# Performance work log

Hardware: AMD Instinct MI355X
Metric: run time of the kernel (lower is better)

Reference implementation:

```python
import jax, jax.numpy as jnp
import numpy as np
import math

B, S, D, H = 2, 2048, 1024, 16
DK = D // H


def setup_inputs() -> dict:
    key = jax.random.key(0)
    ks = jax.random.split(key, 12)
    std = 1.0 / math.sqrt(D)
    inp = {
        "query": jax.random.normal(ks[0], (B, S, D), jnp.float32),
        "key_": jax.random.normal(ks[1], (B, S, D), jnp.float32),
        "value": jax.random.normal(ks[2], (B, S, D), jnp.float32),
        # causal mask: True = masked out
        "attn_mask": jnp.triu(jnp.ones((S, S), jnp.bool_), k=1),
        "w_q": jax.random.uniform(ks[3], (D, D), jnp.float32, -std, std),
        "b_q": jax.random.uniform(ks[4], (D,), jnp.float32, -std, std),
        "w_k": jax.random.uniform(ks[5], (D, D), jnp.float32, -std, std),
        "b_k": jax.random.uniform(ks[6], (D,), jnp.float32, -std, std),
        "w_v": jax.random.uniform(ks[7], (D, D), jnp.float32, -std, std),
        "b_v": jax.random.uniform(ks[8], (D,), jnp.float32, -std, std),
        "w_o": jax.random.uniform(ks[9], (D, D), jnp.float32, -std, std),
        "b_o": jax.random.uniform(ks[10], (D,), jnp.float32, -std, std),
    }
    return inp


def reference(query, key_, value, attn_mask, w_q, b_q, w_k, b_k, w_v, b_v, w_o, b_o):
    # linear projections (torch Linear: x @ W.T + b)
    q = query @ w_q.T + b_q
    k = key_ @ w_k.T + b_k
    v = value @ w_v.T + b_v
    # [B, H, S, DK]
    q = q.reshape(B, S, H, DK).transpose(0, 2, 1, 3)
    k = k.reshape(B, S, H, DK).transpose(0, 2, 1, 3)
    v = v.reshape(B, S, H, DK).transpose(0, 2, 1, 3)
    scores = jnp.einsum("bhqd,bhkd->bhqk", q, k) / jnp.sqrt(jnp.float32(DK))
    scores = jnp.where(attn_mask[None, None, :, :], -jnp.inf, scores)
    attn = jax.nn.softmax(scores, axis=-1)
    context = jnp.einsum("bhqk,bhkd->bhqd", attn, v)
    context = context.transpose(0, 2, 1, 3).reshape(B, S, D)
    return context @ w_o.T + b_o
```

## Files before the change

### kernel.cpp

```cpp
#include <hip/hip_runtime.h>

#define B_ 2
#define S_ 2048
#define D_ 1024
#define H_ 16
#define DK_ 64
#define K_ 1024

typedef __bf16 bf16x8 __attribute__((ext_vector_type(8)));
typedef __bf16 bf16x4 __attribute__((ext_vector_type(4)));
typedef float f32x4 __attribute__((ext_vector_type(4)));

#define QSCALE 0.18033688011112042f

__device__ __forceinline__ void gload16(const void* g, void* l) {
    __builtin_amdgcn_global_load_lds(
        (const __attribute__((address_space(1))) unsigned int*)g,
        (__attribute__((address_space(3))) unsigned int*)l, 16, 0, 0);
}

__device__ __forceinline__ bf16x8 cvt8f(const float* __restrict__ p) {
    f32x4 a = *reinterpret_cast<const f32x4*>(p);
    f32x4 b = *reinterpret_cast<const f32x4*>(p + 4);
    bf16x8 r;
#pragma unroll
    for (int j = 0; j < 4; ++j) { r[j] = (__bf16)a[j]; r[j + 4] = (__bf16)b[j]; }
    return r;
}

__global__ __launch_bounds__(256) void cvt4(
    const float* __restrict__ s0, const float* __restrict__ s1,
    const float* __restrict__ s2, const float* __restrict__ s3,
    __bf16* __restrict__ d0, __bf16* __restrict__ d1,
    __bf16* __restrict__ d2, __bf16* __restrict__ d3, int n8)
{
    const float* s; __bf16* d;
    if (blockIdx.y == 0) { s = s0; d = d0; }
    else if (blockIdx.y == 1) { s = s1; d = d1; }
    else if (blockIdx.y == 2) { s = s2; d = d2; }
    else { s = s3; d = d3; }
    int i = blockIdx.x * 256 + threadIdx.x;
    if (i >= n8) return;
    *reinterpret_cast<bf16x8*>(d + (size_t)i * 8) = cvt8f(s + (size_t)i * 8);
}

__global__ __launch_bounds__(256) void gemm_qkv(
    const float* __restrict__ query, const float* __restrict__ key_, const float* __restrict__ value,
    const __bf16* __restrict__ wq,  const __bf16* __restrict__ wk,  const __bf16* __restrict__ wv,
    const float* __restrict__ bq,   const float* __restrict__ bk,   const float* __restrict__ bv,
    __bf16* __restrict__ qo, __bf16* __restrict__ ko, __bf16* __restrict__ vto)
{
    __shared__ __attribute__((aligned(16))) char ldsF[2][8192];
    __shared__ __attribute__((aligned(16))) char ldsL[2][8192];

    const int tid = threadIdx.x;
    const int w = tid >> 6, lane = tid & 63;
    const int l15 = lane & 15, lh = lane >> 4;
    const int wr = w >> 1, wc = w & 1;

    const int z = blockIdx.z;
    int brow, bcol;
    if (z < 2) { brow = blockIdx.x * 128; bcol = blockIdx.y * 128; }
    else       { brow = (blockIdx.x & 7) * 128; bcol = (blockIdx.y * 4 + (blockIdx.x >> 3)) * 128; }

    const float* Fsrc = (z == 0) ? query : (z == 1) ? key_ : value;
    const int    Frow = (z < 2) ? brow : bcol;
    const char*  Lsrc = (const char*)((z == 0) ? wq : (z == 1) ? wk : wv);
    const int    Lrow = (z < 2) ? bcol : brow;

    const int fr = tid >> 1, fch = tid & 1;
    const float* fbase = Fsrc + (size_t)(Frow + fr) * 1024 + fch * 16;

    const int srow = lane >> 2, scolb = (lane & 3) * 16;

    f32x4 areg[4];
    auto loadF = [&](int k0) {
#pragma unroll
        for (int j = 0; j < 4; ++j)
            areg[j] = *reinterpret_cast<const f32x4*>(fbase + k0 + j * 4);
    };
    auto writeF = [&](int buf) {
        bf16x8 lo, hi;
#pragma unroll
        for (int j = 0; j < 4; ++j) { lo[j] = (__bf16)areg[0][j]; lo[j+4] = (__bf16)areg[1][j];
                                      hi[j] = (__bf16)areg[2][j]; hi[j+4] = (__bf16)areg[3][j]; }
        char* dst = &ldsF[buf][fr * 64 + fch * 32];
        *reinterpret_cast<bf16x8*>(dst) = lo;
        *reinterpret_cast<bf16x8*>(dst + 16) = hi;
    };
    auto stageL = [&](int buf, int k0) {
#pragma unroll
        for (int c = 0; c < 2; ++c) {
            const int chunk = w * 2 + c;
            const int loff  = __builtin_amdgcn_readfirstlane(chunk * 1024);
            gload16(Lsrc + (size_t)(Lrow + chunk * 16 + srow) * 2048 + k0 * 2 + scolb,
                    &ldsL[buf][loff]);
        }
    };

    const char* aLds = (z < 2) ? &ldsF[0][0] : &ldsL[0][0];
    const char* bLds = (z < 2) ? &ldsL[0][0] : &ldsF[0][0];

    f32x4 acc[4][4] = {};
    const int NT = K_ / 32;

    loadF(0); stageL(0, 0);
    asm volatile("s_waitcnt vmcnt(0)" ::: "memory");
    writeF(0);
    loadF(32); stageL(1, 32);
    asm volatile("s_waitcnt lgkmcnt(0)" ::: "memory");
    __builtin_amdgcn_s_barrier();

    for (int t = 0; t < NT; ++t) {
        const int buf = t & 1;
        const int bo  = buf * 8192;

        bf16x8 af[4], bfr[4];
#pragma unroll
        for (int m = 0; m < 4; ++m)
            af[m] = *reinterpret_cast<const bf16x8*>(aLds + bo + (wr * 64 + m * 16 + l15) * 64 + lh * 16);
#pragma unroll
        for (int n = 0; n < 4; ++n)
            bfr[n] = *reinterpret_cast<const bf16x8*>(bLds + bo + (wc * 64 + n * 16 + l15) * 64 + lh * 16);

        __builtin_amdgcn_s_setprio(1);
#pragma unroll
        for (int m = 0; m < 4; ++m)
#pragma unroll
            for (int n = 0; n < 4; ++n)
                acc[m][n] = __builtin_amdgcn_mfma_f32_16x16x32_bf16(af[m], bfr[n], acc[m][n], 0, 0, 0);
        __builtin_amdgcn_s_setprio(0);

        if (t + 1 < NT) {
            asm volatile("s_waitcnt vmcnt(0)" ::: "memory");
            __builtin_amdgcn_s_barrier();
            writeF(buf ^ 1);
            if (t + 2 < NT) { loadF((t + 2) * 32); stageL(buf, (t + 2) * 32); }
            asm volatile("s_waitcnt lgkmcnt(0)" ::: "memory");
            __builtin_amdgcn_s_barrier();
        }
    }

#pragma unroll
    for (int ni = 0; ni < 4; ++ni) {
        const int n = bcol + wc * 64 + ni * 16 + l15;
#pragma unroll
        for (int mi = 0; mi < 4; ++mi)
#pragma unroll
            for (int r = 0; r < 4; ++r) {
                const int m = brow + wr * 64 + mi * 16 + lh * 4 + r;
                if (z < 2) {
                    float v = acc[mi][ni][r] + ((z == 0) ? bq[n] : bk[n]);
                    if (z == 0) v *= QSCALE;
                    const int bb = m >> 11, ss = m & (S_ - 1);
                    const int hh = n >> 6,  dk = n & 63;
                    __bf16* o = (z == 0) ? qo : ko;
                    o[(((size_t)(bb * H_ + hh)) * S_ + ss) * DK_ + dk] = (__bf16)v;
                } else {
                    const float v = acc[mi][ni][r] + bv[m];
                    const int hh = m >> 6,  dk = m & 63;
                    const int bb = n >> 11, ss = n & (S_ - 1);
                    vto[(((size_t)(bb * H_ + hh)) * DK_ + dk) * S_ + ss] = (__bf16)v;
                }
            }
    }
}

__global__ __launch_bounds__(256) void gemm_out(
    const __bf16* __restrict__ A, const __bf16* __restrict__ Bm,
    const float* __restrict__ bias, float* __restrict__ out)
{
    __shared__ __attribute__((aligned(16))) __bf16 ldsA[2 * 128 * 32];
    __shared__ __attribute__((aligned(16))) __bf16 ldsB[2 * 128 * 32];

    const int tid = threadIdx.x;
    const int w = tid >> 6, lane = tid & 63;
    const int l15 = lane & 15, lh = lane >> 4;
    const int wr = w >> 1, wc = w & 1;
    const int brow = blockIdx.x * 128;
    const int bcol = blockIdx.y * 128;
    const int srow  = lane >> 2;
    const int scolb = (lane & 3) * 16;
    const char* Ab = (const char*)A;
    const char* Bb = (const char*)Bm;

    auto stage = [&](int buf, int k0) {
#pragma unroll
        for (int c = 0; c < 2; ++c) {
            const int chunk = w * 2 + c;
            const int row   = chunk * 16 + srow;
            const int loff  = __builtin_amdgcn_readfirstlane(buf * 8192 + chunk * 1024);
            gload16(Ab + (size_t)(brow + row) * 2048 + k0 * 2 + scolb, (char*)ldsA + loff);
            gload16(Bb + (size_t)(bcol + row) * 2048 + k0 * 2 + scolb, (char*)ldsB + loff);
        }
    };

    f32x4 acc[4][4] = {};
    stage(0, 0);
    int buf = 0;
    for (int k0 = 0; k0 < K_; k0 += 32) {
        if (k0 + 32 < K_) {
            stage(buf ^ 1, k0 + 32);
            asm volatile("s_waitcnt vmcnt(4)" ::: "memory");
        } else {
            asm volatile("s_waitcnt vmcnt(0)" ::: "memory");
        }
        __builtin_amdgcn_s_barrier();
        __builtin_amdgcn_sched_barrier(0);

        const int bo = buf * 4096;
        bf16x8 af[4], bfr[4];
#pragma unroll
        for (int m = 0; m < 4; ++m)
            af[m] = *reinterpret_cast<const bf16x8*>(&ldsA[bo + (wr * 64 + m * 16 + l15) * 32 + lh * 8]);
#pragma unroll
        for (int n = 0; n < 4; ++n)
            bfr[n] = *reinterpret_cast<const bf16x8*>(&ldsB[bo + (wc * 64 + n * 16 + l15) * 32 + lh * 8]);

        __builtin_amdgcn_s_setprio(1);
#pragma unroll
        for (int m = 0; m < 4; ++m)
#pragma unroll
            for (int n = 0; n < 4; ++n)
                acc[m][n] = __builtin_amdgcn_mfma_f32_16x16x32_bf16(af[m], bfr[n], acc[m][n], 0, 0, 0);
        __builtin_amdgcn_s_setprio(0);

        __builtin_amdgcn_s_barrier();
        buf ^= 1;
    }

#pragma unroll
    for (int ni = 0; ni < 4; ++ni) {
        const int n = bcol + wc * 64 + ni * 16 + l15;
        const float bv = bias[n];
#pragma unroll
        for (int mi = 0; mi < 4; ++mi)
#pragma unroll
            for (int r = 0; r < 4; ++r) {
                const int m = brow + wr * 64 + mi * 16 + lh * 4 + r;
                out[(size_t)m * D_ + n] = acc[mi][ni][r] + bv;
            }
    }
}

__global__ __launch_bounds__(256, 4) void attn_kernel(
    const __bf16* __restrict__ Q, const __bf16* __restrict__ K,
    const __bf16* __restrict__ VT, __bf16* __restrict__ CTX)
{
    __shared__ __attribute__((aligned(16))) char ldsK[2][8192];
    __shared__ __attribute__((aligned(16))) char ldsV[2][8192];
    __shared__ __attribute__((aligned(16))) __bf16 p_lds[4][16][64];

    const int tid = threadIdx.x;
    const int w = tid >> 6, l = tid & 63;
    const int l15 = l & 15, lh = l >> 4;

    const int c  = blockIdx.x & 255;
    const int rr = blockIdx.x >> 8;
    const int qq = c >> 5;
    const int bhidx = c & 31;
    int panel;
    if (rr == 0)      panel = 31 - qq;
    else if (rr == 1) panel = qq;
    else if (rr == 2) panel = 23 - qq;
    else              panel = 8 + qq;
    const int h = bhidx & 15;
    const int b = bhidx >> 4;

    const size_t bh = (size_t)(b * H_ + h);
    const __bf16* qp   = Q + bh * S_ * DK_;
    const char*  kbase = (const char*)(K  + bh * S_ * DK_);
    const char*  vbase = (const char*)(VT + bh * DK_ * S_);

    const int np = panel + 1;
    const int wave_base = panel * 64 + w * 16;

    const int srow = l >> 3;
    const int ssw  = ((l & 7) * 16) ^ (srow * 16);

    auto stage = [&](int pos) {
        const int k0 = pos * 64;
        char* lk = ldsK[pos & 1];
        char* lv = ldsV[pos & 1];
#pragma unroll
        for (int i = 0; i < 2; ++i) {
            const int r0   = w * 16 + i * 8;
            const int loff = __builtin_amdgcn_readfirstlane(r0 * 128);
            gload16(kbase + (size_t)(k0 + r0 + srow) * 128 + ssw, lk + loff);
            gload16(vbase + (size_t)(r0 + srow) * 4096 + (size_t)k0 * 2 + ssw, lv + loff);
        }
    };

    bf16x8 aq[2];
#pragma unroll
    for (int cc = 0; cc < 2; ++cc)
        aq[cc] = *reinterpret_cast<const bf16x8*>(
            qp + (size_t)(wave_base + l15) * DK_ + cc * 32 + lh * 8);

    bf16x8 vones;
#pragma unroll
    for (int j = 0; j < 8; ++j) vones[j] = (__bf16)1.0f;
    const f32x4 fzero = {0.f, 0.f, 0.f, 0.f};

    f32x4 acc[4] = {};
    f32x4 acc_l = {};
    float mrun = -INFINITY;

    stage(0);

    for (int it = 0; it < np; ++it) {
        if (it + 1 < np) {
            stage(it + 1);
            asm volatile("s_waitcnt vmcnt(4)" ::: "memory");
        } else {
            asm volatile("s_waitcnt vmcnt(0)" ::: "memory");
        }
        __builtin_amdgcn_s_barrier();
        __builtin_amdgcn_sched_barrier(0);

        const int k0 = it * 64;
        const char* lk = ldsK[it & 1];
        const char* lv = ldsV[it & 1];

        bf16x8 ak[4][2];
#pragma unroll
        for (int t = 0; t < 4; ++t)
#pragma unroll
            for (int cc = 0; cc < 2; ++cc) {
                const int col = (cc * 64 + lh * 16) ^ ((l15 & 7) << 4);
                ak[t][cc] = *reinterpret_cast<const bf16x8*>(lk + (t * 16 + l15) * 128 + col);
            }

        f32x4 sacc[4];
        __builtin_amdgcn_s_setprio(1);
#pragma unroll
        for (int t = 0; t < 4; ++t) {
            sacc[t] = __builtin_amdgcn_mfma_f32_16x16x32_bf16(ak[t][0], aq[0], fzero, 0, 0, 0);
            sacc[t] = __builtin_amdgcn_mfma_f32_16x16x32_bf16(ak[t][1], aq[1], sacc[t], 0, 0, 0);
        }
        __builtin_amdgcn_s_setprio(0);

        bf16x8 bv[4][2];
#pragma unroll
        for (int nt = 0; nt < 4; ++nt)
#pragma unroll
            for (int c2 = 0; c2 < 2; ++c2) {
                const int col = (c2 * 64 + lh * 16) ^ ((l15 & 7) << 4);
                bv[nt][c2] = *reinterpret_cast<const bf16x8*>(lv + (nt * 16 + l15) * 128 + col);
            }

        if (k0 + 63 > wave_base) {
            const int qa = wave_base + l15;
#pragma unroll
            for (int t = 0; t < 4; ++t)
#pragma unroll
                for (int r = 0; r < 4; ++r) {
                    const int ka = k0 + t * 16 + lh * 4 + r;
                    if (ka > qa) sacc[t][r] = -INFINITY;
                }
        }

        f32x4 m4 = sacc[0];
#pragma unroll
        for (int t = 1; t < 4; ++t)
#pragma unroll
            for (int r = 0; r < 4; ++r) m4[r] = fmaxf(m4[r], sacc[t][r]);
        float rm = fmaxf(fmaxf(m4[0], m4[1]), fmaxf(m4[2], m4[3]));
        rm = fmaxf(rm, __shfl_xor(rm, 16, 64));
        rm = fmaxf(rm, __shfl_xor(rm, 32, 64));

        if (!__all(rm <= mrun + 8.f)) {
            const float mnew = fmaxf(mrun, rm);
            const float scl  = exp2f(mrun - mnew);
            mrun = mnew;
#pragma unroll
            for (int r = 0; r < 4; ++r) {
                const float sr = __shfl(scl, lh * 4 + r, 64);
#pragma unroll
                for (int nt = 0; nt < 4; ++nt) acc[nt][r] *= sr;
                acc_l[r] *= sr;
            }
        }

#pragma unroll
        for (int t = 0; t < 4; ++t) {
            bf16x4 pk;
#pragma unroll
            for (int r = 0; r < 4; ++r)
                pk[r] = (__bf16)exp2f(sacc[t][r] - mrun);
            const int wcol = (t * 16 + lh * 4) ^ ((l15 & 7) << 3);
            *reinterpret_cast<bf16x4*>(&p_lds[w][l15][wcol]) = pk;
        }

        bf16x8 pa[2];
#pragma unroll
        for (int c2 = 0; c2 < 2; ++c2) {
            const int rcol = (c2 * 32 + lh * 8) ^ ((l15 & 7) << 3);
            pa[c2] = *reinterpret_cast<const bf16x8*>(&p_lds[w][l15][rcol]);
        }

        __builtin_amdgcn_s_setprio(1);
#pragma unroll
        for (int nt = 0; nt < 4; ++nt)
#pragma unroll
            for (int c2 = 0; c2 < 2; ++c2)
                acc[nt] = __builtin_amdgcn_mfma_f32_16x16x32_bf16(
                    pa[c2], bv[nt][c2], acc[nt], 0, 0, 0);
        acc_l = __builtin_amdgcn_mfma_f32_16x16x32_bf16(pa[0], vones, acc_l, 0, 0, 0);
        acc_l = __builtin_amdgcn_mfma_f32_16x16x32_bf16(pa[1], vones, acc_l, 0, 0, 0);
        __builtin_amdgcn_s_setprio(0);

        __builtin_amdgcn_s_barrier();
    }

#pragma unroll
    for (int r = 0; r < 4; ++r) {
        const float linv = 1.f / acc_l[r];
        const int srow2 = wave_base + lh * 4 + r;
#pragma unroll
        for (int nt = 0; nt < 4; ++nt)
            CTX[((size_t)b * S_ + srow2) * D_ + h * DK_ + nt * 16 + l15] =
                (__bf16)(acc[nt][r] * linv);
    }
}

extern "C" void kernel_launch(void* const* d_in, const int* in_sizes, int n_in,
                              void* d_out, int out_size, void* d_ws, size_t ws_size,
                              hipStream_t stream) {
    (void)in_sizes; (void)n_in; (void)out_size; (void)ws_size;

    const float* query = (const float*)d_in[0];
    const float* key_  = (const float*)d_in[1];
    const float* value = (const float*)d_in[2];
    const float* w_q = (const float*)d_in[4];
    const float* b_q = (const float*)d_in[5];
    const float* w_k = (const float*)d_in[6];
    const float* b_k = (const float*)d_in[7];
    const float* w_v = (const float*)d_in[8];
    const float* b_v = (const float*)d_in[9];
    const float* w_o = (const float*)d_in[10];
    const float* b_o = (const float*)d_in[11];
    float* out = (float*)d_out;

    char* Wp = (char*)d_ws;
    const size_t MB = 1024 * 1024;
    __bf16* ctx = (__bf16*)(Wp + 0 * MB);
    __bf16* wq  = (__bf16*)(Wp + 24 * MB);
    __bf16* wk  = (__bf16*)(Wp + 26 * MB);
    __bf16* wv  = (__bf16*)(Wp + 28 * MB);
    __bf16* wo  = (__bf16*)(Wp + 30 * MB);
    __bf16* q   = (__bf16*)(Wp + 32 * MB);
    __bf16* k   = (__bf16*)(Wp + 40 * MB);
    __bf16* vt  = (__bf16*)(Wp + 48 * MB);

    const int n8_w = (D_ * D_) / 8;

    hipLaunchKernelGGL(cvt4, dim3(n8_w / 256, 4), dim3(256), 0, stream,
                       w_q, w_k, w_v, w_o, wq, wk, wv, wo, n8_w);
    hipLaunchKernelGGL(gemm_qkv, dim3(32, 8, 3), dim3(256), 0, stream,
                       query, key_, value, wq, wk, wv, b_q, b_k, b_v, q, k, vt);
    hipLaunchKernelGGL(attn_kernel, dim3(1024), dim3(256), 0, stream,
                       q, k, vt, ctx);
    hipLaunchKernelGGL(gemm_out, dim3(32, 8), dim3(256), 0, stream,
                       ctx, wo, b_o, out);
}
```

Baseline: 134.7 us.

## Pre-convert activations to bf16 and use direct-to-LDS loads for both GEMM operands

```diff
diff --git a/kernel.cpp b/kernel.cpp
--- a/kernel.cpp
+++ b/kernel.cpp
@@ -28,100 +28,90 @@
     return r;
 }
 
-__global__ __launch_bounds__(256) void cvt4(
-    const float* __restrict__ s0, const float* __restrict__ s1,
-    const float* __restrict__ s2, const float* __restrict__ s3,
-    __bf16* __restrict__ d0, __bf16* __restrict__ d1,
-    __bf16* __restrict__ d2, __bf16* __restrict__ d3, int n8)
+__global__ __launch_bounds__(256) void cvt_all(
+    const float* __restrict__ s0, const float* __restrict__ s1, const float* __restrict__ s2,
+    const float* __restrict__ s3, const float* __restrict__ s4, const float* __restrict__ s5,
+    const float* __restrict__ s6,
+    __bf16* __restrict__ d0, __bf16* __restrict__ d1, __bf16* __restrict__ d2,
+    __bf16* __restrict__ d3, __bf16* __restrict__ d4, __bf16* __restrict__ d5,
+    __bf16* __restrict__ d6)
 {
-    const float* s; __bf16* d;
-    if (blockIdx.y == 0) { s = s0; d = d0; }
-    else if (blockIdx.y == 1) { s = s1; d = d1; }
-    else if (blockIdx.y == 2) { s = s2; d = d2; }
-    else { s = s3; d = d3; }
+    const int y = blockIdx.y;
+    const float* s; __bf16* d; int n8;
+    const int n8_big = (B_ * S_ * D_) / 8, n8_w = (D_ * D_) / 8;
+    switch (y) {
+        case 0: s = s0; d = d0; n8 = n8_big; break;
+        case 1: s = s1; d = d1; n8 = n8_big; break;
+        case 2: s = s2; d = d2; n8 = n8_big; break;
+        case 3: s = s3; d = d3; n8 = n8_w; break;
+        case 4: s = s4; d = d4; n8 = n8_w; break;
+        case 5: s = s5; d = d5; n8 = n8_w; break;
+        default: s = s6; d = d6; n8 = n8_w; break;
+    }
     int i = blockIdx.x * 256 + threadIdx.x;
     if (i >= n8) return;
     *reinterpret_cast<bf16x8*>(d + (size_t)i * 8) = cvt8f(s + (size_t)i * 8);
 }
 
 __global__ __launch_bounds__(256) void gemm_qkv(
-    const float* __restrict__ query, const float* __restrict__ key_, const float* __restrict__ value,
+    const __bf16* __restrict__ qin, const __bf16* __restrict__ kin, const __bf16* __restrict__ vin,
     const __bf16* __restrict__ wq,  const __bf16* __restrict__ wk,  const __bf16* __restrict__ wv,
     const float* __restrict__ bq,   const float* __restrict__ bk,   const float* __restrict__ bv,
     __bf16* __restrict__ qo, __bf16* __restrict__ ko, __bf16* __restrict__ vto)
 {
-    __shared__ __attribute__((aligned(16))) char ldsF[2][8192];
-    __shared__ __attribute__((aligned(16))) char ldsL[2][8192];
+    __shared__ __attribute__((aligned(16))) __bf16 ldsA[2 * 128 * 32];
+    __shared__ __attribute__((aligned(16))) __bf16 ldsB[2 * 128 * 32];
+
+    const int z = blockIdx.z;
+    const __bf16* A; const __bf16* Bm;
+    int brow, bcol;
+    if (z == 0)      { A = qin; Bm = wq;  brow = blockIdx.x * 128; bcol = blockIdx.y * 128; }
+    else if (z == 1) { A = kin; Bm = wk;  brow = blockIdx.x * 128; bcol = blockIdx.y * 128; }
+    else             { A = wv;  Bm = vin;
+                       brow = (blockIdx.x & 7) * 128;
+                       bcol = (blockIdx.y * 4 + (blockIdx.x >> 3)) * 128; }
 
     const int tid = threadIdx.x;
     const int w = tid >> 6, lane = tid & 63;
     const int l15 = lane & 15, lh = lane >> 4;
     const int wr = w >> 1, wc = w & 1;
-
-    const int z = blockIdx.z;
-    int brow, bcol;
-    if (z < 2) { brow = blockIdx.x * 128; bcol = blockIdx.y * 128; }
-    else       { brow = (blockIdx.x & 7) * 128; bcol = (blockIdx.y * 4 + (blockIdx.x >> 3)) * 128; }
-
-    const float* Fsrc = (z == 0) ? query : (z == 1) ? key_ : value;
-    const int    Frow = (z < 2) ? brow : bcol;
-    const char*  Lsrc = (const char*)((z == 0) ? wq : (z == 1) ? wk : wv);
-    const int    Lrow = (z < 2) ? bcol : brow;
-
-    const int fr = tid >> 1, fch = tid & 1;
-    const float* fbase = Fsrc + (size_t)(Frow + fr) * 1024 + fch * 16;
-
-    const int srow = lane >> 2, scolb = (lane & 3) * 16;
-
-    f32x4 areg[4];
-    auto loadF = [&](int k0) {
-#pragma unroll
-        for (int j = 0; j < 4; ++j)
-            areg[j] = *reinterpret_cast<const f32x4*>(fbase + k0 + j * 4);
-    };
-    auto writeF = [&](int buf) {
-        bf16x8 lo, hi;
-#pragma unroll
-        for (int j = 0; j < 4; ++j) { lo[j] = (__bf16)areg[0][j]; lo[j+4] = (__bf16)areg[1][j];
-                                      hi[j] = (__bf16)areg[2][j]; hi[j+4] = (__bf16)areg[3][j]; }
-        char* dst = &ldsF[buf][fr * 64 + fch * 32];
-        *reinterpret_cast<bf16x8*>(dst) = lo;
-        *reinterpret_cast<bf16x8*>(dst + 16) = hi;
-    };
-    auto stageL = [&](int buf, int k0) {
+    const int srow  = lane >> 2;
+    const int scolb = (lane & 3) * 16;
+    const char* Ab = (const char*)A;
+    const char* Bb = (const char*)Bm;
+
+    auto stage = [&](int buf, int k0) {
 #pragma unroll
         for (int c = 0; c < 2; ++c) {
             const int chunk = w * 2 + c;
-            const int loff  = __builtin_amdgcn_readfirstlane(chunk * 1024);
-            gload16(Lsrc + (size_t)(Lrow + chunk * 16 + srow) * 2048 + k0 * 2 + scolb,
-                    &ldsL[buf][loff]);
+            const int row   = chunk * 16 + srow;
+            const int loff  = __builtin_amdgcn_readfirstlane(buf * 8192 + chunk * 1024);
+            gload16(Ab + (size_t)(brow + row) * 2048 + k0 * 2 + scolb, (char*)ldsA + loff);
+            gload16(Bb + (size_t)(bcol + row) * 2048 + k0 * 2 + scolb, (char*)ldsB + loff);
         }
     };
 
-    const char* aLds = (z < 2) ? &ldsF[0][0] : &ldsL[0][0];
-    const char* bLds = (z < 2) ? &ldsL[0][0] : &ldsF[0][0];
-
     f32x4 acc[4][4] = {};
-    const int NT = K_ / 32;
-
-    loadF(0); stageL(0, 0);
-    asm volatile("s_waitcnt vmcnt(0)" ::: "memory");
-    writeF(0);
-    loadF(32); stageL(1, 32);
-    asm volatile("s_waitcnt lgkmcnt(0)" ::: "memory");
-    __builtin_amdgcn_s_barrier();
-
-    for (int t = 0; t < NT; ++t) {
-        const int buf = t & 1;
-        const int bo  = buf * 8192;
-
+    stage(0, 0);
+    int buf = 0;
+    for (int k0 = 0; k0 < K_; k0 += 32) {
+        if (k0 + 32 < K_) {
+            stage(buf ^ 1, k0 + 32);
+            asm volatile("s_waitcnt vmcnt(4)" ::: "memory");
+        } else {
+            asm volatile("s_waitcnt vmcnt(0)" ::: "memory");
+        }
+        __builtin_amdgcn_s_barrier();
+        __builtin_amdgcn_sched_barrier(0);
+
+        const int bo = buf * 4096;
         bf16x8 af[4], bfr[4];
 #pragma unroll
         for (int m = 0; m < 4; ++m)
-            af[m] = *reinterpret_cast<const bf16x8*>(aLds + bo + (wr * 64 + m * 16 + l15) * 64 + lh * 16);
+            af[m] = *reinterpret_cast<const bf16x8*>(&ldsA[bo + (wr * 64 + m * 16 + l15) * 32 + lh * 8]);
 #pragma unroll
         for (int n = 0; n < 4; ++n)
-            bfr[n] = *reinterpret_cast<const bf16x8*>(bLds + bo + (wc * 64 + n * 16 + l15) * 64 + lh * 16);
+            bfr[n] = *reinterpret_cast<const bf16x8*>(&ldsB[bo + (wc * 64 + n * 16 + l15) * 32 + lh * 8]);
 
         __builtin_amdgcn_s_setprio(1);
 #pragma unroll
@@ -131,14 +121,8 @@
                 acc[m][n] = __builtin_amdgcn_mfma_f32_16x16x32_bf16(af[m], bfr[n], acc[m][n], 0, 0, 0);
         __builtin_amdgcn_s_setprio(0);
 
-        if (t + 1 < NT) {
-            asm volatile("s_waitcnt vmcnt(0)" ::: "memory");
-            __builtin_amdgcn_s_barrier();
-            writeF(buf ^ 1);
-            if (t + 2 < NT) { loadF((t + 2) * 32); stageL(buf, (t + 2) * 32); }
-            asm volatile("s_waitcnt lgkmcnt(0)" ::: "memory");
-            __builtin_amdgcn_s_barrier();
-        }
+        __builtin_amdgcn_s_barrier();
+        buf ^= 1;
     }
 
 #pragma unroll
@@ -232,13 +216,13 @@
 #pragma unroll
     for (int ni = 0; ni < 4; ++ni) {
         const int n = bcol + wc * 64 + ni * 16 + l15;
-        const float bv = bias[n];
+        const float bvv = bias[n];
 #pragma unroll
         for (int mi = 0; mi < 4; ++mi)
 #pragma unroll
             for (int r = 0; r < 4; ++r) {
                 const int m = brow + wr * 64 + mi * 16 + lh * 4 + r;
-                out[(size_t)m * D_ + n] = acc[mi][ni][r] + bv;
+                out[(size_t)m * D_ + n] = acc[mi][ni][r] + bvv;
             }
     }
 }
@@ -444,7 +428,9 @@
 
     char* Wp = (char*)d_ws;
     const size_t MB = 1024 * 1024;
-    __bf16* ctx = (__bf16*)(Wp + 0 * MB);
+    __bf16* qin = (__bf16*)(Wp + 0 * MB);
+    __bf16* kin = (__bf16*)(Wp + 8 * MB);
+    __bf16* vin = (__bf16*)(Wp + 16 * MB);
     __bf16* wq  = (__bf16*)(Wp + 24 * MB);
     __bf16* wk  = (__bf16*)(Wp + 26 * MB);
     __bf16* wv  = (__bf16*)(Wp + 28 * MB);
@@ -452,13 +438,15 @@
     __bf16* q   = (__bf16*)(Wp + 32 * MB);
     __bf16* k   = (__bf16*)(Wp + 40 * MB);
     __bf16* vt  = (__bf16*)(Wp + 48 * MB);
-
-    const int n8_w = (D_ * D_) / 8;
-
-    hipLaunchKernelGGL(cvt4, dim3(n8_w / 256, 4), dim3(256), 0, stream,
-                       w_q, w_k, w_v, w_o, wq, wk, wv, wo, n8_w);
+    __bf16* ctx = qin;
+
+    const int n8_big = (B_ * S_ * D_) / 8;
+
+    hipLaunchKernelGGL(cvt_all, dim3(n8_big / (256 * 8) * 8, 7), dim3(256), 0, stream,
+                       query, key_, value, w_q, w_k, w_v, w_o,
+                       qin, kin, vin, wq, wk, wv, wo);
     hipLaunchKernelGGL(gemm_qkv, dim3(32, 8, 3), dim3(256), 0, stream,
-                       query, key_, value, wq, wk, wv, b_q, b_k, b_v, q, k, vt);
+                       qin, kin, vin, wq, wk, wv, b_q, b_k, b_v, q, k, vt);
     hipLaunchKernelGGL(attn_kernel, dim3(1024), dim3(256), 0, stream,
                        q, k, vt, ctx);
     hipLaunchKernelGGL(gemm_out, dim3(32, 8), dim3(256), 0, stream,
```

Result: faster. 128.5 us (-4.6%).
